# Kernel tuning notes

Hardware: AMD Instinct MI355X
Metric: run time of the kernel (lower is better)

Reference implementation:

```python
import jax, jax.numpy as jnp
import numpy as np

N_USER = 100000
N_ITEM = 100000
N_EDGE = 1000000
IN_DIM = 256
HID = 128
OUT = 16
LEAKY_SLOPE = 0.01  # torch F.leaky_relu default


def _seg_mean(msg, dst, num_segments):
    # segment mean with zero in-degree -> 0 (DGL mean semantics)
    s = jax.ops.segment_sum(msg, dst, num_segments=num_segments)
    c = jax.ops.segment_sum(jnp.ones((dst.shape[0], 1), msg.dtype), dst, num_segments=num_segments)
    return jnp.where(c > 0, s / jnp.maximum(c, 1.0), 0.0)


def setup_inputs() -> dict:
    key = jax.random.key(0)
    ks = jax.random.split(key, 24)
    def lin(k, fan_in, fan_out):
        # torch nn.Linear init: U(-1/sqrt(fan_in), 1/sqrt(fan_in)) for W and b
        bound = 1.0 / np.sqrt(fan_in)
        kw, kb = jax.random.split(k)
        W = jax.random.uniform(kw, (fan_in, fan_out), jnp.float32, -bound, bound)
        b = jax.random.uniform(kb, (fan_out,), jnp.float32, -bound, bound)
        return W, b
    inp = {}
    inp['feat_user'] = jax.random.normal(ks[0], (N_USER, IN_DIM), jnp.float32)
    inp['feat_item'] = jax.random.normal(ks[1], (N_ITEM, IN_DIM), jnp.float32)
    inp['src_clicks'] = jax.random.randint(ks[2], (N_EDGE,), 0, N_USER, jnp.int32)
    inp['dst_clicks'] = jax.random.randint(ks[3], (N_EDGE,), 0, N_ITEM, jnp.int32)
    inp['src_cb'] = jax.random.randint(ks[4], (N_EDGE,), 0, N_ITEM, jnp.int32)
    inp['dst_cb'] = jax.random.randint(ks[5], (N_EDGE,), 0, N_USER, jnp.int32)
    inp['Win_user'], inp['bin_user'] = lin(ks[6], IN_DIM, HID)
    inp['Win_item'], inp['bin_item'] = lin(ks[7], IN_DIM, HID)
    inp['W0_clicks'], inp['b0_clicks'] = lin(ks[8], HID, HID)
    inp['W0_cb'], inp['b0_cb'] = lin(ks[9], HID, HID)
    inp['W1_clicks'], inp['b1_clicks'] = lin(ks[10], HID, HID)
    inp['W1_cb'], inp['b1_cb'] = lin(ks[11], HID, HID)
    inp['Wout'], inp['bout'] = lin(ks[12], HID, OUT)
    return inp


def reference(feat_user, feat_item, src_clicks, dst_clicks, src_cb, dst_cb,
              Win_user, bin_user, Win_item, bin_item,
              W0_clicks, b0_clicks, W0_cb, b0_cb,
              W1_clicks, b1_clicks, W1_cb, b1_cb,
              Wout, bout):
    # input projections per node type
    x_u = feat_user @ Win_user + bin_user   # [N_USER, HID]
    x_i = feat_item @ Win_item + bin_item   # [N_ITEM, HID]

    def layer(x_u, x_i, Wc, bc, Wcb, bcb):
        # per-relation Linear on source nodes, then copy_u gather + mean scatter
        wh_u = x_u @ Wc + bc                 # user -> clicks -> item
        wh_i = x_i @ Wcb + bcb               # item -> clicked_by -> user
        h_i = _seg_mean(wh_u[src_clicks], dst_clicks, N_ITEM)
        h_u = _seg_mean(wh_i[src_cb], dst_cb, N_USER)
        return h_u, h_i

    h_u, h_i = layer(x_u, x_i, W0_clicks, b0_clicks, W0_cb, b0_cb)
    h_u = jax.nn.leaky_relu(h_u, LEAKY_SLOPE)
    h_i = jax.nn.leaky_relu(h_i, LEAKY_SLOPE)
    h_u, h_i = layer(h_u, h_i, W1_clicks, b1_clicks, W1_cb, b1_cb)

    # final projection on target_node = 'user'
    return h_u @ Wout + bout
```

## Files before the change

kernel.cpp:

```cpp
#include <hip/hip_runtime.h>
#include <hip/hip_bf16.h>
#include <cstddef>
#include <cstdint>

#define N_USER 100000
#define N_ITEM 100000
#define N_EDGE 1000000
#define IN_DIM 256
#define HID 128
#define OUT_DIM 16
#define LEAKY_SLOPE 0.01f
#define SRC_MASK 0x07FFFFFFu

#define NC 98
#define CAPB 12288
#define TILE 4096
#define GP 245
#define GM 782

typedef __attribute__((ext_vector_type(8))) short bf16x8;
typedef __attribute__((ext_vector_type(4))) float f32x4;

static __device__ __forceinline__ unsigned short f2bf(float f) {
  unsigned int u = __float_as_uint(f);
  u = (u + 0x7FFFu + ((u >> 16) & 1u)) >> 16;
  return (unsigned short)u;
}

static __device__ __forceinline__ void split8(const float4 x, const float4 y,
                                              bf16x8& hi, bf16x8& lo) {
  const float f[8] = {x.x, x.y, x.z, x.w, y.x, y.y, y.z, y.w};
#pragma unroll
  for (int j = 0; j < 8; ++j) {
    const unsigned u = __float_as_uint(f[j]);
    hi[j] = (short)(u >> 16);
    const float lf = f[j] - __uint_as_float(u & 0xffff0000u);
    lo[j] = (short)(__float_as_uint(lf) >> 16);
  }
}

union P1Shared {
  struct {
    uint32_t srec[TILE];
    unsigned char sbkt[TILE];
    int hist[NC], lofs[NC], gbase[NC], lcur[NC];
  } a;
  float wsbuf[HID * OUT_DIM];
};

static __device__ void part_coarse_body(const int* __restrict__ src,
                                        const int* __restrict__ dst,
                                        int* __restrict__ gcur,
                                        uint32_t* __restrict__ tmp,
                                        int y, int b, P1Shared& S) {
  const int t = threadIdx.x;
  const int e0 = b * TILE;
  const int ne = min(TILE, N_EDGE - e0);

  for (int i = t; i < NC; i += 256) S.a.hist[i] = 0;
  __syncthreads();

  uint32_t rec[16];
  int bk[16];
#pragma unroll
  for (int q = 0; q < 16; ++q) {
    const int i = t + q * 256;
    if (i < ne) {
      const int d = dst[e0 + i];
      rec[q] = (uint32_t)src[e0 + i] | ((uint32_t)(d & 1023) << 17);
      bk[q] = d >> 10;
      atomicAdd(&S.a.hist[bk[q]], 1);
    } else {
      bk[q] = -1;
    }
  }
  __syncthreads();

  if (t == 0) {
    int run = 0;
#pragma unroll 1
    for (int i = 0; i < NC; ++i) { S.a.lofs[i] = run; run += S.a.hist[i]; }
  }
  __syncthreads();
  if (t < NC) {
    S.a.lcur[t] = 0;
    S.a.gbase[t] = atomicAdd(&gcur[y * NC + t], S.a.hist[t]);
  }
  __syncthreads();

#pragma unroll
  for (int q = 0; q < 16; ++q) {
    if (bk[q] >= 0) {
      const int p = S.a.lofs[bk[q]] + atomicAdd(&S.a.lcur[bk[q]], 1);
      S.a.srec[p] = rec[q];
      S.a.sbkt[p] = (unsigned char)bk[q];
    }
  }
  __syncthreads();

  uint32_t* __restrict__ outp = tmp + (size_t)y * NC * CAPB;
  for (int i = t; i < ne; i += 256) {
    const int b2 = S.a.sbkt[i];
    outp[(size_t)b2 * CAPB + S.a.gbase[b2] + (i - S.a.lofs[b2])] = S.a.srec[i];
  }
}

static __device__ void make_wfuse0_body(const float* __restrict__ Win,
                                        const float* __restrict__ bin,
                                        const float* __restrict__ W0,
                                        const float* __restrict__ b0,
                                        unsigned short* __restrict__ Bswz,
                                        float* __restrict__ bf0, int bx) {
  const int t = threadIdx.x;
  const int r = bx * 2 + (t >> 7);
  const int n = t & 127;
  const float* wr = Win + (size_t)r * HID;
  float s = 0.f;
#pragma unroll 8
  for (int m = 0; m < HID; ++m) s += wr[m] * W0[(size_t)m * HID + n];
  const unsigned u = __float_as_uint(s);
  const unsigned short hi = (unsigned short)(u >> 16);
  const float lf = s - __uint_as_float(u & 0xffff0000u);
  const unsigned short lo = (unsigned short)(__float_as_uint(lf) >> 16);
  const int kt = r >> 5, lh = (r >> 3) & 3, j = r & 7;
  const int nf = n >> 4, lane = lh * 16 + (n & 15);
  Bswz[(size_t)(kt * 16 + nf * 2) * 512 + lane * 8 + j] = hi;
  Bswz[(size_t)(kt * 16 + nf * 2 + 1) * 512 + lane * 8 + j] = lo;
  if (bx == 0 && t < HID) {
    float s2 = b0[t];
    for (int m = 0; m < HID; ++m) s2 += bin[m] * W0[(size_t)m * HID + t];
    bf0[t] = s2;
  }
}

static __device__ void make_wfuse_body(const float* __restrict__ W1,
                                       const float* __restrict__ b1,
                                       const float* __restrict__ Wout,
                                       const float* __restrict__ bout,
                                       float* __restrict__ Wf,
                                       float* __restrict__ bf, P1Shared& S) {
  const int t = threadIdx.x;
  {
    const float4* s0 = (const float4*)Wout;
    float4* dp = (float4*)S.wsbuf;
    dp[t]       = s0[t];
    dp[t + 256] = s0[t + 256];
  }
  __syncthreads();
  const int k  = t >> 1;
  const int j0 = (t & 1) * 8;
  const float* w1row = W1 + (size_t)k * HID;
  float acc[8] = {0.f, 0.f, 0.f, 0.f, 0.f, 0.f, 0.f, 0.f};
  for (int m = 0; m < HID; ++m) {
    const float a = w1row[m];
    const float* wr = &S.wsbuf[m * OUT_DIM + j0];
#pragma unroll
    for (int q = 0; q < 8; ++q) acc[q] += a * wr[q];
  }
#pragma unroll
  for (int q = 0; q < 8; ++q) Wf[(size_t)k * OUT_DIM + j0 + q] = acc[q];
  if (t < OUT_DIM) {
    float s = bout[t];
    for (int m = 0; m < HID; ++m) s += b1[m] * S.wsbuf[m * OUT_DIM + t];
    bf[t] = s;
  }
}

__global__ __launch_bounds__(256)
void prep1(const int* __restrict__ srcA, const int* __restrict__ dstA,
           const int* __restrict__ srcB, const int* __restrict__ dstB,
           int* __restrict__ gcur, uint32_t* __restrict__ tmp,
           const float* __restrict__ Win, const float* __restrict__ bin,
           const float* __restrict__ W0, const float* __restrict__ b0,
           unsigned short* __restrict__ Bswz, float* __restrict__ bf0,
           const float* __restrict__ W1, const float* __restrict__ b1,
           const float* __restrict__ Wout, const float* __restrict__ bout,
           float* __restrict__ Wf, float* __restrict__ bf) {
  __shared__ P1Shared S;
  const int bx = blockIdx.x;
  if (bx < 2 * GP) {
    const int y = bx >= GP ? 1 : 0;
    part_coarse_body(y ? srcB : srcA, y ? dstB : dstA, gcur, tmp, y, bx - y * GP, S);
  } else if (bx < 2 * GP + 128) {
    make_wfuse0_body(Win, bin, W0, b0, Bswz, bf0, bx - 2 * GP);
  } else {
    make_wfuse_body(W1, b1, Wout, bout, Wf, bf, S);
  }
}

__global__ __launch_bounds__(256)
void part_fine(const uint32_t* __restrict__ tmp, const int* __restrict__ gcur,
               uint32_t* __restrict__ ebuf, int* __restrict__ pos,
               int* __restrict__ cnt) {
  __shared__ int dcnt[1024];
  __shared__ int sh[256];
  const int y = blockIdx.y, b = blockIdx.x, t = threadIdx.x;
  const int ne = gcur[y * NC + b];
  const uint32_t* __restrict__ in = tmp + ((size_t)y * NC + b) * CAPB;

  for (int i = t; i < 1024; i += 256) dcnt[i] = 0;
  __syncthreads();
  for (int i = t; i < ne; i += 256) atomicAdd(&dcnt[in[i] >> 17], 1);
  __syncthreads();

  const int bi = t * 4;
  const int v0 = dcnt[bi], v1 = dcnt[bi + 1], v2 = dcnt[bi + 2], v3 = dcnt[bi + 3];
  const int tsum = v0 + v1 + v2 + v3;
  sh[t] = tsum;
  __syncthreads();
#pragma unroll
  for (int d = 1; d < 256; d <<= 1) {
    const int x = (t >= d) ? sh[t - d] : 0;
    __syncthreads();
    sh[t] += x;
    __syncthreads();
  }
  const int p0 = sh[t] - tsum;
  const int p1 = p0 + v0, p2 = p1 + v1, p3 = p2 + v2;
  dcnt[bi] = p0; dcnt[bi + 1] = p1; dcnt[bi + 2] = p2; dcnt[bi + 3] = p3;

  const int drow0 = (b << 10) + bi;
  const int prel = b * CAPB;
  int* __restrict__ cw = cnt + (size_t)y * N_USER;
  int* __restrict__ pw = pos + (size_t)y * N_USER;
  if (drow0 + 0 < N_USER) { cw[drow0 + 0] = v0; pw[drow0 + 0] = prel + p0; }
  if (drow0 + 1 < N_USER) { cw[drow0 + 1] = v1; pw[drow0 + 1] = prel + p1; }
  if (drow0 + 2 < N_USER) { cw[drow0 + 2] = v2; pw[drow0 + 2] = prel + p2; }
  if (drow0 + 3 < N_USER) { cw[drow0 + 3] = v3; pw[drow0 + 3] = prel + p3; }
  __syncthreads();

  uint32_t* __restrict__ outp = ebuf + ((size_t)y * NC + b) * CAPB;
  for (int i = t; i < ne; i += 256) {
    const uint32_t r = in[i];
    const int p = atomicAdd(&dcnt[r >> 17], 1);
    outp[p] = r & 0x1FFFFu;
  }
}

__global__ __launch_bounds__(256, 4)
void gemm_feat_mfma(const float* __restrict__ A,
                    const unsigned short* __restrict__ Bswz,
                    const float* __restrict__ bias,
                    unsigned short* __restrict__ Wh, int M) {
  __shared__ unsigned short Bs[2][8192];
  const int t = threadIdx.x;
  const int w = t >> 6, lane = t & 63;
  const int rowW = blockIdx.x * 128 + w * 32;
  const int lr = lane & 15;
  const int lk = (lane >> 4) << 3;

  int r0 = rowW + lr;      if (r0 >= M) r0 = M - 1;
  int r1 = rowW + 16 + lr; if (r1 >= M) r1 = M - 1;
  const float* pa0 = A + (size_t)r0 * IN_DIM + lk;
  const float* pa1 = A + (size_t)r1 * IN_DIM + lk;

  f32x4 acc[2][8];
#pragma unroll
  for (int rf = 0; rf < 2; ++rf)
#pragma unroll
    for (int nf = 0; nf < 8; ++nf)
#pragma unroll
      for (int q = 0; q < 4; ++q) acc[rf][nf][q] = 0.f;

  float4 af[2][2][2];

#define STAGE_B(c, buf)                                                        \
  {                                                                            \
    _Pragma("unroll")                                                          \
    for (int i = 0; i < 4; ++i)                                                \
      __builtin_amdgcn_global_load_lds(                                        \
          (const __attribute__((address_space(1))) unsigned int*)              \
              ((const char*)Bswz + (c) * 16384 + i * 4096 + t * 16),           \
          (__attribute__((address_space(3))) unsigned int*)                    \
              &Bs[buf][i * 2048 + w * 512],                                    \
          16, 0, 0);                                                           \
  }

#define LOAD_A(c, buf)                                                         \
  {                                                                            \
    af[buf][0][0] = *(const float4*)(pa0 + (c) * 32);                          \
    af[buf][0][1] = *(const float4*)(pa0 + (c) * 32 + 4);                      \
    af[buf][1][0] = *(const float4*)(pa1 + (c) * 32);                          \
    af[buf][1][1] = *(const float4*)(pa1 + (c) * 32 + 4);                      \
  }

  STAGE_B(0, 0)
  LOAD_A(0, 0)
  __syncthreads();

#pragma unroll
  for (int c = 0; c < 8; ++c) {
    const int cb = c & 1;
    if (c < 7) {
      STAGE_B(c + 1, cb ^ 1)
      LOAD_A(c + 1, cb ^ 1)
    }
    bf16x8 ah[2], al[2];
#pragma unroll
    for (int rf = 0; rf < 2; ++rf)
      split8(af[cb][rf][0], af[cb][rf][1], ah[rf], al[rf]);
#pragma unroll
    for (int nf = 0; nf < 8; ++nf) {
      const bf16x8 bh = *(const bf16x8*)&Bs[cb][(nf * 2) * 512 + lane * 8];
      const bf16x8 bl = *(const bf16x8*)&Bs[cb][(nf * 2 + 1) * 512 + lane * 8];
#pragma unroll
      for (int rf = 0; rf < 2; ++rf) {
        acc[rf][nf] = __builtin_amdgcn_mfma_f32_16x16x32_bf16(
            ah[rf], bh, acc[rf][nf], 0, 0, 0);
        acc[rf][nf] = __builtin_amdgcn_mfma_f32_16x16x32_bf16(
            ah[rf], bl, acc[rf][nf], 0, 0, 0);
        acc[rf][nf] = __builtin_amdgcn_mfma_f32_16x16x32_bf16(
            al[rf], bh, acc[rf][nf], 0, 0, 0);
      }
    }
    __syncthreads();
  }
#undef STAGE_B
#undef LOAD_A

  float bv[8];
#pragma unroll
  for (int nf = 0; nf < 8; ++nf) bv[nf] = bias[nf * 16 + lr];

#pragma unroll
  for (int rf = 0; rf < 2; ++rf) {
#pragma unroll
    for (int i = 0; i < 4; ++i) {
      const int row = rowW + rf * 16 + ((lane >> 4) << 2) + i;
      if (row < M) {
        unsigned short* op = Wh + (size_t)row * HID + lr;
#pragma unroll
        for (int nf = 0; nf < 8; ++nf) op[nf * 16] = f2bf(acc[rf][nf][i] + bv[nf]);
      }
    }
  }
}

static __device__ __forceinline__ void acc_bf8(float* a, uint4 u) {
  a[0] += __uint_as_float(u.x << 16);
  a[1] += __uint_as_float(u.x & 0xffff0000u);
  a[2] += __uint_as_float(u.y << 16);
  a[3] += __uint_as_float(u.y & 0xffff0000u);
  a[4] += __uint_as_float(u.z << 16);
  a[5] += __uint_as_float(u.z & 0xffff0000u);
  a[6] += __uint_as_float(u.w << 16);
  a[7] += __uint_as_float(u.w & 0xffff0000u);
}

__global__ __launch_bounds__(256)
void gather_z_fused2(const unsigned short* __restrict__ bh,
                     const int* __restrict__ pos, const int* __restrict__ cnt,
                     const uint32_t* __restrict__ ebuf,
                     const float* __restrict__ Wf, float* __restrict__ z) {
  __shared__ float hs[16 * 132];
  __shared__ float ws[HID * OUT_DIM];
  const int t = threadIdx.x;
  {
    const float4* s0 = (const float4*)Wf;
    float4* dp = (float4*)ws;
    dp[t]       = s0[t];
    dp[t + 256] = s0[t + 256];
  }
  const int r = t >> 4;
  const int c = t & 15;
  const int row = blockIdx.x * 16 + r;
  const int beg = pos[row];
  const int cn  = cnt[row];
  float acc[8] = {0.f, 0.f, 0.f, 0.f, 0.f, 0.f, 0.f, 0.f};
  int i = 0;
  for (; i + 8 <= cn; i += 8) {
    int s[8];
#pragma unroll
    for (int q = 0; q < 8; ++q) s[q] = (int)(ebuf[beg + i + q] & SRC_MASK);
    uint4 v[8];
#pragma unroll
    for (int q = 0; q < 8; ++q) v[q] = *((const uint4*)(bh + (size_t)s[q] * HID) + c);
#pragma unroll
    for (int q = 0; q < 8; ++q) acc_bf8(acc, v[q]);
  }
  for (; i + 4 <= cn; i += 4) {
    int s[4];
#pragma unroll
    for (int q = 0; q < 4; ++q) s[q] = (int)(ebuf[beg + i + q] & SRC_MASK);
    uint4 v[4];
#pragma unroll
    for (int q = 0; q < 4; ++q) v[q] = *((const uint4*)(bh + (size_t)s[q] * HID) + c);
#pragma unroll
    for (int q = 0; q < 4; ++q) acc_bf8(acc, v[q]);
  }
  for (; i < cn; ++i) {
    const int s = (int)(ebuf[beg + i] & SRC_MASK);
    const uint4 v = *((const uint4*)(bh + (size_t)s * HID) + c);
    acc_bf8(acc, v);
  }
  const float inv = cn > 0 ? 1.0f / (float)cn : 0.0f;
  float h[8];
#pragma unroll
  for (int q = 0; q < 8; ++q) {
    float v = acc[q] * inv;
    h[q] = v > 0.f ? v : LEAKY_SLOPE * v;
  }
  *(float4*)&hs[r * 132 + c * 8]     = make_float4(h[0], h[1], h[2], h[3]);
  *(float4*)&hs[r * 132 + c * 8 + 4] = make_float4(h[4], h[5], h[6], h[7]);
  __syncthreads();
  const int j = c;
  float s = 0.f;
  const float* hp = &hs[r * 132];
#pragma unroll 8
  for (int k = 0; k < HID; ++k) s += hp[k] * ws[k * OUT_DIM + j];
  z[(size_t)row * OUT_DIM + j] = s;
}

__global__ __launch_bounds__(256)
void gather_mean16(const float* __restrict__ z, const int* __restrict__ pos,
                   const int* __restrict__ cnt, const uint32_t* __restrict__ ebuf,
                   const float* __restrict__ bfuse, const float* __restrict__ bout,
                   float* __restrict__ out) {
  const int row = blockIdx.x * 16 + (threadIdx.x >> 4);
  const int c = threadIdx.x & 15;
  const int beg = pos[row];
  const int cn  = cnt[row];
  float acc = 0.f;
  int i = 0;
  for (; i + 8 <= cn; i += 8) {
    int s[8];
#pragma unroll
    for (int q = 0; q < 8; ++q) s[q] = (int)(ebuf[beg + i + q] & SRC_MASK);
    float v[8];
#pragma unroll
    for (int q = 0; q < 8; ++q) v[q] = z[(size_t)s[q] * OUT_DIM + c];
#pragma unroll
    for (int q = 0; q < 8; ++q) acc += v[q];
  }
  for (; i + 4 <= cn; i += 4) {
    int s[4];
#pragma unroll
    for (int q = 0; q < 4; ++q) s[q] = (int)(ebuf[beg + i + q] & SRC_MASK);
    float v[4];
#pragma unroll
    for (int q = 0; q < 4; ++q) v[q] = z[(size_t)s[q] * OUT_DIM + c];
#pragma unroll
    for (int q = 0; q < 4; ++q) acc += v[q];
  }
  for (; i < cn; ++i) {
    const int s = (int)(ebuf[beg + i] & SRC_MASK);
    acc += z[(size_t)s * OUT_DIM + c];
  }
  float o;
  if (cn > 0) o = acc * (1.0f / (float)cn) + bfuse[c];
  else        o = bout[c];
  out[(size_t)row * OUT_DIM + c] = o;
}

extern "C" void kernel_launch(void* const* d_in, const int* in_sizes, int n_in,
                              void* d_out, int out_size, void* d_ws, size_t ws_size,
                              hipStream_t stream) {
  const float* feat_user  = (const float*)d_in[0];
  const int*   src_clicks = (const int*)d_in[2];
  const int*   dst_clicks = (const int*)d_in[3];
  const int*   src_cb     = (const int*)d_in[4];
  const int*   dst_cb     = (const int*)d_in[5];
  const float* Win_user   = (const float*)d_in[6];
  const float* bin_user   = (const float*)d_in[7];
  const float* W0_clicks  = (const float*)d_in[10];
  const float* b0_clicks  = (const float*)d_in[11];
  const float* W1_cb      = (const float*)d_in[16];
  const float* b1_cb      = (const float*)d_in[17];
  const float* Wout       = (const float*)d_in[18];
  const float* bout       = (const float*)d_in[19];
  float* out = (float*)d_out;

  const size_t SZ  = (size_t)N_USER * HID * sizeof(float);
  const size_t SZH = (size_t)N_USER * HID * sizeof(unsigned short);
  const size_t SZZ = (size_t)N_USER * OUT_DIM * sizeof(float);
  char* ws = (char*)d_ws;
  uint32_t* tmp        = (uint32_t*)ws;
  unsigned short* bh   = (unsigned short*)(ws + SZ);
  float* z0            = (float*)(ws + SZ + SZH);
  unsigned short* Bswz = (unsigned short*)z0;
  float* bf0v          = (float*)((char*)z0 + 131072);
  float* Wf            = (float*)(ws + SZ + SZH + SZZ);
  float* bf            = Wf + HID * OUT_DIM;
  int* cnt  = (int*)(bf + OUT_DIM);
  int* pos  = cnt + 2 * N_USER;
  int* gcur = pos + 2 * N_USER;
  uint32_t* ebuf = (uint32_t*)(gcur + 2 * NC + 12);

  const int G16 = N_USER / 16;

  hipMemsetAsync(gcur, 0, (size_t)2 * NC * sizeof(int), stream);
  prep1<<<2 * GP + 128 + 1, 256, 0, stream>>>(
      src_clicks, dst_clicks, src_cb, dst_cb, gcur, tmp,
      Win_user, bin_user, W0_clicks, b0_clicks, Bswz, bf0v,
      W1_cb, b1_cb, Wout, bout, Wf, bf);
  part_fine<<<dim3(NC, 2), 256, 0, stream>>>(tmp, gcur, ebuf, pos, cnt);
  gemm_feat_mfma<<<GM, 256, 0, stream>>>(feat_user, Bswz, bf0v, bh, N_USER);
  gather_z_fused2<<<G16, 256, 0, stream>>>(bh, pos, cnt, ebuf, Wf, z0);
  gather_mean16<<<G16, 256, 0, stream>>>(z0, pos + N_USER, cnt + N_USER,
                                         ebuf + (size_t)NC * CAPB, bf, bout, out);
}
```

Measured before the change: 361.0 us.

## Hold GEMM weight fragments in registers and split output columns across waves

```diff
diff --git a/kernel.cpp b/kernel.cpp
--- a/kernel.cpp
+++ b/kernel.cpp
@@ -16,7 +16,7 @@
 #define CAPB 12288
 #define TILE 4096
 #define GP 245
-#define GM 782
+#define GM32 3125
 
 typedef __attribute__((ext_vector_type(8))) short bf16x8;
 typedef __attribute__((ext_vector_type(4))) float f32x4;
@@ -237,15 +237,14 @@
   }
 }
 
-__global__ __launch_bounds__(256, 4)
+__global__ __launch_bounds__(256, 2)
 void gemm_feat_mfma(const float* __restrict__ A,
                     const unsigned short* __restrict__ Bswz,
                     const float* __restrict__ bias,
                     unsigned short* __restrict__ Wh, int M) {
-  __shared__ unsigned short Bs[2][8192];
   const int t = threadIdx.x;
   const int w = t >> 6, lane = t & 63;
-  const int rowW = blockIdx.x * 128 + w * 32;
+  const int rowW = blockIdx.x * 32;
   const int lr = lane & 15;
   const int lk = (lane >> 4) << 3;
 
@@ -254,27 +253,25 @@
   const float* pa0 = A + (size_t)r0 * IN_DIM + lk;
   const float* pa1 = A + (size_t)r1 * IN_DIM + lk;
 
-  f32x4 acc[2][8];
+  bf16x8 bfr[2][8][2];
+#pragma unroll
+  for (int kt = 0; kt < 8; ++kt)
+#pragma unroll
+    for (int j = 0; j < 2; ++j)
+#pragma unroll
+      for (int s = 0; s < 2; ++s)
+        bfr[j][kt][s] = *(const bf16x8*)&Bswz[
+            (size_t)(kt * 16 + (2 * w + j) * 2 + s) * 512 + lane * 8];
+
+  f32x4 acc[2][2];
 #pragma unroll
   for (int rf = 0; rf < 2; ++rf)
 #pragma unroll
-    for (int nf = 0; nf < 8; ++nf)
-#pragma unroll
-      for (int q = 0; q < 4; ++q) acc[rf][nf][q] = 0.f;
+    for (int j = 0; j < 2; ++j)
+#pragma unroll
+      for (int q = 0; q < 4; ++q) acc[rf][j][q] = 0.f;
 
   float4 af[2][2][2];
-
-#define STAGE_B(c, buf)                                                        \
-  {                                                                            \
-    _Pragma("unroll")                                                          \
-    for (int i = 0; i < 4; ++i)                                                \
-      __builtin_amdgcn_global_load_lds(                                        \
-          (const __attribute__((address_space(1))) unsigned int*)              \
-              ((const char*)Bswz + (c) * 16384 + i * 4096 + t * 16),           \
-          (__attribute__((address_space(3))) unsigned int*)                    \
-              &Bs[buf][i * 2048 + w * 512],                                    \
-          16, 0, 0);                                                           \
-  }
 
 #define LOAD_A(c, buf)                                                         \
   {                                                                            \
@@ -284,43 +281,36 @@
     af[buf][1][1] = *(const float4*)(pa1 + (c) * 32 + 4);                      \
   }
 
-  STAGE_B(0, 0)
   LOAD_A(0, 0)
-  __syncthreads();
 
 #pragma unroll
   for (int c = 0; c < 8; ++c) {
     const int cb = c & 1;
-    if (c < 7) {
-      STAGE_B(c + 1, cb ^ 1)
-      LOAD_A(c + 1, cb ^ 1)
-    }
+    if (c < 7) LOAD_A(c + 1, cb ^ 1)
     bf16x8 ah[2], al[2];
 #pragma unroll
     for (int rf = 0; rf < 2; ++rf)
       split8(af[cb][rf][0], af[cb][rf][1], ah[rf], al[rf]);
 #pragma unroll
-    for (int nf = 0; nf < 8; ++nf) {
-      const bf16x8 bh = *(const bf16x8*)&Bs[cb][(nf * 2) * 512 + lane * 8];
-      const bf16x8 bl = *(const bf16x8*)&Bs[cb][(nf * 2 + 1) * 512 + lane * 8];
+    for (int j = 0; j < 2; ++j) {
+      const bf16x8 bh = bfr[j][c][0];
+      const bf16x8 bl = bfr[j][c][1];
 #pragma unroll
       for (int rf = 0; rf < 2; ++rf) {
-        acc[rf][nf] = __builtin_amdgcn_mfma_f32_16x16x32_bf16(
-            ah[rf], bh, acc[rf][nf], 0, 0, 0);
-        acc[rf][nf] = __builtin_amdgcn_mfma_f32_16x16x32_bf16(
-            ah[rf], bl, acc[rf][nf], 0, 0, 0);
-        acc[rf][nf] = __builtin_amdgcn_mfma_f32_16x16x32_bf16(
-            al[rf], bh, acc[rf][nf], 0, 0, 0);
+        acc[rf][j] = __builtin_amdgcn_mfma_f32_16x16x32_bf16(
+            ah[rf], bh, acc[rf][j], 0, 0, 0);
+        acc[rf][j] = __builtin_amdgcn_mfma_f32_16x16x32_bf16(
+            ah[rf], bl, acc[rf][j], 0, 0, 0);
+        acc[rf][j] = __builtin_amdgcn_mfma_f32_16x16x32_bf16(
+            al[rf], bh, acc[rf][j], 0, 0, 0);
       }
     }
-    __syncthreads();
-  }
-#undef STAGE_B
+  }
 #undef LOAD_A
 
-  float bv[8];
-#pragma unroll
-  for (int nf = 0; nf < 8; ++nf) bv[nf] = bias[nf * 16 + lr];
+  float bv[2];
+#pragma unroll
+  for (int j = 0; j < 2; ++j) bv[j] = bias[w * 32 + j * 16 + lr];
 
 #pragma unroll
   for (int rf = 0; rf < 2; ++rf) {
@@ -328,9 +318,9 @@
     for (int i = 0; i < 4; ++i) {
       const int row = rowW + rf * 16 + ((lane >> 4) << 2) + i;
       if (row < M) {
-        unsigned short* op = Wh + (size_t)row * HID + lr;
-#pragma unroll
-        for (int nf = 0; nf < 8; ++nf) op[nf * 16] = f2bf(acc[rf][nf][i] + bv[nf]);
+        unsigned short* op = Wh + (size_t)row * HID + w * 32 + lr;
+#pragma unroll
+        for (int j = 0; j < 2; ++j) op[j * 16] = f2bf(acc[rf][j][i] + bv[j]);
       }
     }
   }
@@ -494,7 +484,7 @@
       Win_user, bin_user, W0_clicks, b0_clicks, Bswz, bf0v,
       W1_cb, b1_cb, Wout, bout, Wf, bf);
   part_fine<<<dim3(NC, 2), 256, 0, stream>>>(tmp, gcur, ebuf, pos, cnt);
-  gemm_feat_mfma<<<GM, 256, 0, stream>>>(feat_user, Bswz, bf0v, bh, N_USER);
+  gemm_feat_mfma<<<GM32, 256, 0, stream>>>(feat_user, Bswz, bf0v, bh, N_USER);
   gather_z_fused2<<<G16, 256, 0, stream>>>(bh, pos, cnt, ebuf, Wf, z0);
   gather_mean16<<<G16, 256, 0, stream>>>(z0, pos + N_USER, cnt + N_USER,
                                          ebuf + (size_t)NC * CAPB, bf, bout, out);
```

Measured after the change: 386.9 us. 7.2% more time.

## Deepen input-projection GEMM pipeline to four-slot staging with fewer barriers

Applied to the files above, without the earlier changes.

```diff
diff --git a/kernel.cpp b/kernel.cpp
--- a/kernel.cpp
+++ b/kernel.cpp
@@ -237,12 +237,12 @@
   }
 }
 
-__global__ __launch_bounds__(256, 4)
+__global__ __launch_bounds__(256, 2)
 void gemm_feat_mfma(const float* __restrict__ A,
                     const unsigned short* __restrict__ Bswz,
                     const float* __restrict__ bias,
                     unsigned short* __restrict__ Wh, int M) {
-  __shared__ unsigned short Bs[2][8192];
+  __shared__ unsigned short Bs[4][8192];
   const int t = threadIdx.x;
   const int w = t >> 6, lane = t & 63;
   const int rowW = blockIdx.x * 128 + w * 32;
@@ -262,9 +262,9 @@
 #pragma unroll
       for (int q = 0; q < 4; ++q) acc[rf][nf][q] = 0.f;
 
-  float4 af[2][2][2];
-
-#define STAGE_B(c, buf)                                                        \
+  float4 af[4][2][2];
+
+#define STAGE_B(c, slot)                                                       \
   {                                                                            \
     _Pragma("unroll")                                                          \
     for (int i = 0; i < 4; ++i)                                                \
@@ -272,51 +272,66 @@
           (const __attribute__((address_space(1))) unsigned int*)              \
               ((const char*)Bswz + (c) * 16384 + i * 4096 + t * 16),           \
           (__attribute__((address_space(3))) unsigned int*)                    \
-              &Bs[buf][i * 2048 + w * 512],                                    \
+              &Bs[slot][i * 2048 + w * 512],                                   \
           16, 0, 0);                                                           \
   }
 
-#define LOAD_A(c, buf)                                                         \
+#define LOAD_A(c, slot)                                                        \
   {                                                                            \
-    af[buf][0][0] = *(const float4*)(pa0 + (c) * 32);                          \
-    af[buf][0][1] = *(const float4*)(pa0 + (c) * 32 + 4);                      \
-    af[buf][1][0] = *(const float4*)(pa1 + (c) * 32);                          \
-    af[buf][1][1] = *(const float4*)(pa1 + (c) * 32 + 4);                      \
-  }
-
-  STAGE_B(0, 0)
-  LOAD_A(0, 0)
-  __syncthreads();
-
-#pragma unroll
-  for (int c = 0; c < 8; ++c) {
-    const int cb = c & 1;
-    if (c < 7) {
-      STAGE_B(c + 1, cb ^ 1)
-      LOAD_A(c + 1, cb ^ 1)
-    }
-    bf16x8 ah[2], al[2];
-#pragma unroll
-    for (int rf = 0; rf < 2; ++rf)
-      split8(af[cb][rf][0], af[cb][rf][1], ah[rf], al[rf]);
-#pragma unroll
-    for (int nf = 0; nf < 8; ++nf) {
-      const bf16x8 bh = *(const bf16x8*)&Bs[cb][(nf * 2) * 512 + lane * 8];
-      const bf16x8 bl = *(const bf16x8*)&Bs[cb][(nf * 2 + 1) * 512 + lane * 8];
-#pragma unroll
-      for (int rf = 0; rf < 2; ++rf) {
-        acc[rf][nf] = __builtin_amdgcn_mfma_f32_16x16x32_bf16(
-            ah[rf], bh, acc[rf][nf], 0, 0, 0);
-        acc[rf][nf] = __builtin_amdgcn_mfma_f32_16x16x32_bf16(
-            ah[rf], bl, acc[rf][nf], 0, 0, 0);
-        acc[rf][nf] = __builtin_amdgcn_mfma_f32_16x16x32_bf16(
-            al[rf], bh, acc[rf][nf], 0, 0, 0);
-      }
-    }
-    __syncthreads();
-  }
+    af[slot][0][0] = *(const float4*)(pa0 + (c) * 32);                         \
+    af[slot][0][1] = *(const float4*)(pa0 + (c) * 32 + 4);                     \
+    af[slot][1][0] = *(const float4*)(pa1 + (c) * 32);                         \
+    af[slot][1][1] = *(const float4*)(pa1 + (c) * 32 + 4);                     \
+  }
+
+#define COMPUTE(slotA, slotB)                                                  \
+  {                                                                            \
+    bf16x8 ah[2], al[2];                                                       \
+    _Pragma("unroll")                                                          \
+    for (int rf = 0; rf < 2; ++rf)                                             \
+      split8(af[slotA][rf][0], af[slotA][rf][1], ah[rf], al[rf]);              \
+    _Pragma("unroll")                                                          \
+    for (int nf = 0; nf < 8; ++nf) {                                           \
+      const bf16x8 bh = *(const bf16x8*)&Bs[slotB][(nf * 2) * 512 + lane * 8]; \
+      const bf16x8 bl = *(const bf16x8*)&Bs[slotB][(nf * 2 + 1) * 512 + lane * 8]; \
+      _Pragma("unroll")                                                        \
+      for (int rf = 0; rf < 2; ++rf) {                                         \
+        acc[rf][nf] = __builtin_amdgcn_mfma_f32_16x16x32_bf16(                 \
+            ah[rf], bh, acc[rf][nf], 0, 0, 0);                                 \
+        acc[rf][nf] = __builtin_amdgcn_mfma_f32_16x16x32_bf16(                 \
+            ah[rf], bl, acc[rf][nf], 0, 0, 0);                                 \
+        acc[rf][nf] = __builtin_amdgcn_mfma_f32_16x16x32_bf16(                 \
+            al[rf], bh, acc[rf][nf], 0, 0, 0);                                 \
+      }                                                                        \
+    }                                                                          \
+  }
+
+  STAGE_B(0, 0) STAGE_B(1, 1) STAGE_B(2, 2) STAGE_B(3, 3)
+  LOAD_A(0, 0) LOAD_A(1, 1) LOAD_A(2, 2)
+  __syncthreads();
+
+  LOAD_A(3, 3)
+  COMPUTE(0, 0)
+  LOAD_A(4, 0)
+  COMPUTE(1, 1)
+  LOAD_A(5, 1)
+  COMPUTE(2, 2)
+  LOAD_A(6, 2)
+  COMPUTE(3, 3)
+  LOAD_A(7, 3)
+
+  __syncthreads();
+  STAGE_B(4, 0) STAGE_B(5, 1) STAGE_B(6, 2) STAGE_B(7, 3)
+  __syncthreads();
+
+  COMPUTE(0, 0)
+  COMPUTE(1, 1)
+  COMPUTE(2, 2)
+  COMPUTE(3, 3)
+
 #undef STAGE_B
 #undef LOAD_A
+#undef COMPUTE
 
   float bv[8];
 #pragma unroll
```

Result: no change. 367.4 us (+1.8%).
